# Performance work log

Hardware: AMD Instinct MI355X
Metric: run time of the kernel (lower is better)

The kernel has to match this reference:

```python
import jax, jax.numpy as jnp
import numpy as np

N_NODES = 50000


def _sage_conv(x, src, dst, W_l, b_l, W_r):
    # PyG SAGEConv (aggr='mean'): out = lin_l(mean_{j in N(i)} x_j) + lin_r(x_i)
    # lin_l has bias, lin_r has no bias.
    neigh_sum = jax.ops.segment_sum(x[src], dst, num_segments=N_NODES)  # [N, F]
    deg = jax.ops.segment_sum(jnp.ones_like(dst, dtype=x.dtype), dst, num_segments=N_NODES)
    neigh_mean = neigh_sum / jnp.maximum(deg, 1.0)[:, None]
    return neigh_mean @ W_l.T + b_l + x @ W_r.T


def setup_inputs() -> dict:
    key = jax.random.key(0)
    ks = jax.random.split(key, 8)
    D, H, C = 768, 128, 4
    x = jax.random.normal(ks[0], (N_NODES, D), dtype=jnp.float32)
    edge_index = jax.random.randint(ks[1], (2, 800000), 0, N_NODES, dtype=jnp.int64)
    s1 = 1.0 / np.sqrt(D)
    s2 = 1.0 / np.sqrt(H)
    return {
        "x": x,
        "edge_index": edge_index,
        "W1_l": jax.random.uniform(ks[2], (H, D), jnp.float32, -s1, s1),
        "b1_l": jnp.zeros((H,), jnp.float32),
        "W1_r": jax.random.uniform(ks[3], (H, D), jnp.float32, -s1, s1),
        "W2_l": jax.random.uniform(ks[4], (C, H), jnp.float32, -s2, s2),
        "b2_l": jnp.zeros((C,), jnp.float32),
        "W2_r": jax.random.uniform(ks[5], (C, H), jnp.float32, -s2, s2),
    }


def reference(x, edge_index, W1_l, b1_l, W1_r, W2_l, b2_l, W2_r):
    src, dst = edge_index[0], edge_index[1]
    h = jax.nn.relu(_sage_conv(x, src, dst, W1_l, b1_l, W1_r))  # [N, H]
    out = _sage_conv(h, src, dst, W2_l, b2_l, W2_r)  # [N, C]
    return out
```

## Files before the change

### kernel.cpp

```cpp
#include <hip/hip_runtime.h>


typedef __bf16 bf16x8 __attribute__((ext_vector_type(8)));
typedef float  f32x4  __attribute__((ext_vector_type(4)));

__device__ __forceinline__ float bf16_lo(uint32_t w) {
    union { uint32_t u; float f; } c; c.u = w << 16; return c.f;
}
__device__ __forceinline__ float bf16_hi(uint32_t w) {
    union { uint32_t u; float f; } c; c.u = w & 0xffff0000u; return c.f;
}

__global__ __launch_bounds__(256)
void convert_w(const float* __restrict__ W1l, const float* __restrict__ W1r,
               __bf16* __restrict__ Wb)
{
    int i = blockIdx.x * 256 + threadIdx.x;
    if (i >= 256 * 768) return;
    int n = i / 768, k = i - n * 768;
    float v = (n < 128) ? W1l[n * 768 + k] : W1r[(n - 128) * 768 + k];
    Wb[i] = (__bf16)v;
}

__global__ __launch_bounds__(512)
void gemm_bf16(const float* __restrict__ A, const __bf16* __restrict__ Bw,
               __bf16* __restrict__ Cb, int M)
{
    constexpr int LDK = 72;
    __shared__ __bf16 As[64][LDK];
    __shared__ __bf16 Bs[256][LDK];
    const int bm   = blockIdx.x * 64;
    const int tid  = threadIdx.x;
    const int lane = tid & 63;
    const int wave = tid >> 6;
    const int wr = wave >> 2, wc = wave & 3;
    const int l15 = lane & 15;
    const int lk  = lane >> 4;

    f32x4 acc[2][4] = {};
    float4 apref[2];
    bf16x8 bpref[4];

    const int arow = tid >> 3;
    const int akc  = (tid & 7) << 3;

    auto load_tile = [&](int k0) {
        if (bm + arow < M) {
            const float* src = A + (size_t)(bm + arow) * 768 + k0 + akc;
            apref[0] = *(const float4*)src;
            apref[1] = *(const float4*)(src + 4);
        } else {
            apref[0] = make_float4(0.f, 0.f, 0.f, 0.f);
            apref[1] = make_float4(0.f, 0.f, 0.f, 0.f);
        }
        #pragma unroll
        for (int it = 0; it < 4; ++it) {
            int v = it * 512 + tid;
            int row = v >> 3, kc = (v & 7) << 3;
            bpref[it] = *(const bf16x8*)(Bw + (size_t)row * 768 + k0 + kc);
        }
    };

    load_tile(0);
    for (int kt = 0; kt < 12; ++kt) {
        if (kt) __syncthreads();
        {
            float4 f0 = apref[0], f1 = apref[1];
            bf16x8 b;
            b[0] = (__bf16)f0.x; b[1] = (__bf16)f0.y;
            b[2] = (__bf16)f0.z; b[3] = (__bf16)f0.w;
            b[4] = (__bf16)f1.x; b[5] = (__bf16)f1.y;
            b[6] = (__bf16)f1.z; b[7] = (__bf16)f1.w;
            *(bf16x8*)&As[arow][akc] = b;
        }
        #pragma unroll
        for (int it = 0; it < 4; ++it) {
            int v = it * 512 + tid;
            int row = v >> 3, kc = (v & 7) << 3;
            *(bf16x8*)&Bs[row][kc] = bpref[it];
        }
        __syncthreads();
        if (kt < 11) load_tile((kt + 1) * 64);

        #pragma unroll
        for (int ks = 0; ks < 2; ++ks) {
            int koff = ks * 32 + lk * 8;
            bf16x8 af[2], bfr[4];
            #pragma unroll
            for (int i = 0; i < 2; ++i)
                af[i] = *(const bf16x8*)&As[wr * 32 + i * 16 + l15][koff];
            #pragma unroll
            for (int j = 0; j < 4; ++j)
                bfr[j] = *(const bf16x8*)&Bs[wc * 64 + j * 16 + l15][koff];
            #pragma unroll
            for (int i = 0; i < 2; ++i)
                #pragma unroll
                for (int j = 0; j < 4; ++j)
                    acc[i][j] = __builtin_amdgcn_mfma_f32_16x16x32_bf16(
                        af[i], bfr[j], acc[i][j], 0, 0, 0);
        }
    }

    #pragma unroll
    for (int i = 0; i < 2; ++i)
        #pragma unroll
        for (int j = 0; j < 4; ++j)
            #pragma unroll
            for (int v = 0; v < 4; ++v) {
                int row = bm + wr * 32 + i * 16 + lk * 4 + v;
                int col = wc * 64 + j * 16 + l15;
                if (row < M) Cb[(size_t)row * 256 + col] = (__bf16)acc[i][j][v];
            }
}

__global__ __launch_bounds__(256)
void zero_deg(int* __restrict__ deg, int N)
{
    int i = blockIdx.x * 256 + threadIdx.x;
    if (i < N) deg[i] = 0;
}

__global__ __launch_bounds__(256)
void csr_count(const int* __restrict__ ei, int* __restrict__ deg, int E)
{
    int e = blockIdx.x * 256 + threadIdx.x;
    if (e >= E) return;
    atomicAdd(&deg[ei[E + e]], 1);
}

__global__ __launch_bounds__(1024)
void scan1(const int* __restrict__ deg, int* __restrict__ row_ptr,
           int* __restrict__ partials, int N)
{
    __shared__ int buf[1024];
    int i = blockIdx.x * 1024 + threadIdx.x;
    int v = (i < N) ? deg[i] : 0;
    int val = v;
    buf[threadIdx.x] = val;
    __syncthreads();
    for (int off = 1; off < 1024; off <<= 1) {
        int t = (threadIdx.x >= (unsigned)off) ? buf[threadIdx.x - off] : 0;
        __syncthreads();
        val += t;
        buf[threadIdx.x] = val;
        __syncthreads();
    }
    if (i < N) row_ptr[i] = val - v;
    if (threadIdx.x == 1023) partials[blockIdx.x] = val;
}

__global__ __launch_bounds__(64)
void scan2(int* __restrict__ partials, int nb, int* __restrict__ row_ptr,
           int N, int E)
{
    int lane = threadIdx.x;
    int v = (lane < nb) ? partials[lane] : 0;
    int s = v;
    #pragma unroll
    for (int off = 1; off < 64; off <<= 1) {
        int t = __shfl_up(s, off);
        if (lane >= off) s += t;
    }
    if (lane < nb) partials[lane] = s - v;
    if (lane == 0) row_ptr[N] = E;
}

__global__ __launch_bounds__(1024)
void scan3(int* __restrict__ row_ptr, int* __restrict__ cursor,
           const int* __restrict__ partials, int N)
{
    int i = blockIdx.x * 1024 + threadIdx.x;
    if (i >= N) return;
    int v = row_ptr[i] + partials[blockIdx.x];
    row_ptr[i] = v;
    cursor[i]  = v;
}

__global__ __launch_bounds__(256)
void csr_fill(const int* __restrict__ ei, int* __restrict__ cursor,
              int* __restrict__ csr_src, int E)
{
    int e = blockIdx.x * 256 + threadIdx.x;
    if (e >= E) return;
    int src = ei[e];
    int dst = ei[E + e];
    int pos = atomicAdd(&cursor[dst], 1);
    csr_src[pos] = src;
}

__global__ __launch_bounds__(256)
void sage1_fused(const int* __restrict__ row_ptr, const int* __restrict__ csr_src,
                 const __bf16* __restrict__ pq, const float* __restrict__ b1,
                 const float* __restrict__ W2l, const float* __restrict__ W2r,
                 float* __restrict__ r, float* __restrict__ s, int N)
{
    __shared__ float Wl[512], Wr[512];
    for (int i = threadIdx.x; i < 512; i += 256) {
        Wl[i] = W2l[i];
        Wr[i] = W2r[i];
    }
    __syncthreads();

    int wid  = threadIdx.x >> 6;
    int lane = threadIdx.x & 63;
    int g = lane >> 4;
    int l = lane & 15;
    int n = blockIdx.x * 4 + wid;
    if (n >= N) return;
    int beg = row_ptr[n], end = row_ptr[n + 1];

    float acc8[8] = {};
    for (int eb = beg; eb < end; eb += 64) {
        int cnt = min(64, end - eb);
        int id = (eb + lane < end) ? csr_src[eb + lane] : 0;
        for (int t = 0; t < cnt; t += 4) {
            int src = __shfl(id, t + g);
            if (t + g < cnt) {
                uint4 w = *(const uint4*)(pq + (size_t)src * 256 + l * 8);
                acc8[0] += bf16_lo(w.x); acc8[1] += bf16_hi(w.x);
                acc8[2] += bf16_lo(w.y); acc8[3] += bf16_hi(w.y);
                acc8[4] += bf16_lo(w.z); acc8[5] += bf16_hi(w.z);
                acc8[6] += bf16_lo(w.w); acc8[7] += bf16_hi(w.w);
            }
        }
    }
    #pragma unroll
    for (int c = 0; c < 8; ++c) {
        acc8[c] += __shfl_xor(acc8[c], 16);
        acc8[c] += __shfl_xor(acc8[c], 32);
    }

    float inv = 1.0f / fmaxf((float)(end - beg), 1.0f);
    uint4  qw  = *(const uint4*)(pq + (size_t)n * 256 + 128 + l * 8);
    float4 bv0 = *(const float4*)(b1 + l * 8);
    float4 bv1 = *(const float4*)(b1 + l * 8 + 4);
    float h[8];
    h[0] = fmaxf(acc8[0] * inv + bv0.x + bf16_lo(qw.x), 0.f);
    h[1] = fmaxf(acc8[1] * inv + bv0.y + bf16_hi(qw.x), 0.f);
    h[2] = fmaxf(acc8[2] * inv + bv0.z + bf16_lo(qw.y), 0.f);
    h[3] = fmaxf(acc8[3] * inv + bv0.w + bf16_hi(qw.y), 0.f);
    h[4] = fmaxf(acc8[4] * inv + bv1.x + bf16_lo(qw.z), 0.f);
    h[5] = fmaxf(acc8[5] * inv + bv1.y + bf16_hi(qw.z), 0.f);
    h[6] = fmaxf(acc8[6] * inv + bv1.z + bf16_lo(qw.w), 0.f);
    h[7] = fmaxf(acc8[7] * inv + bv1.w + bf16_hi(qw.w), 0.f);

    float part[8];
    #pragma unroll
    for (int c = 0; c < 4; ++c) {
        float pl = 0.f, pr = 0.f;
        #pragma unroll
        for (int j = 0; j < 8; ++j) {
            pl = fmaf(h[j], Wl[c * 128 + l * 8 + j], pl);
            pr = fmaf(h[j], Wr[c * 128 + l * 8 + j], pr);
        }
        part[c] = pl; part[4 + c] = pr;
    }
    #pragma unroll
    for (int off = 8; off; off >>= 1)
        #pragma unroll
        for (int c = 0; c < 8; ++c)
            part[c] += __shfl_xor(part[c], off);
    if (lane == 0) {
        *(float4*)(r + (size_t)n * 4) = make_float4(part[0], part[1], part[2], part[3]);
        *(float4*)(s + (size_t)n * 4) = make_float4(part[4], part[5], part[6], part[7]);
    }
}

__global__ __launch_bounds__(256)
void sage2_gather(const int* __restrict__ row_ptr, const int* __restrict__ csr_src,
                  const float* __restrict__ r, const float* __restrict__ s,
                  const float* __restrict__ b2, float* __restrict__ out, int N)
{
    int t = blockIdx.x * 256 + threadIdx.x;
    if (t >= N * 4) return;
    int n = t >> 2, c = t & 3;
    int beg = row_ptr[n], end = row_ptr[n + 1];
    float acc = 0.f;
    for (int e = beg; e < end; ++e)
        acc += r[(size_t)csr_src[e] * 4 + c];
    out[t] = acc / fmaxf((float)(end - beg), 1.0f) + b2[c] + s[t];
}

extern "C" void kernel_launch(void* const* d_in, const int* in_sizes, int n_in,
                              void* d_out, int out_size, void* d_ws, size_t ws_size,
                              hipStream_t stream)
{
    const float* x   = (const float*)d_in[0];
    const int*   ei  = (const int*)d_in[1];
    const float* W1l = (const float*)d_in[2];
    const float* b1l = (const float*)d_in[3];
    const float* W1r = (const float*)d_in[4];
    const float* W2l = (const float*)d_in[5];
    const float* b2l = (const float*)d_in[6];
    const float* W2r = (const float*)d_in[7];
    float* out = (float*)d_out;

    const int N = in_sizes[0] / 768;
    const int E = in_sizes[1] / 2;
    const int NB = (N + 1023) / 1024;

    char* ws = (char*)d_ws;
    size_t off = 0;
    auto alloc = [&](size_t bytes) -> void* {
        void* pp = ws + off;
        off += (bytes + 255) & ~(size_t)255;
        return pp;
    };
    __bf16* pq      = (__bf16*)alloc((size_t)N * 256 * 2);
    float*  r       = (float*)alloc((size_t)N * 4 * 4);
    float*  s       = (float*)alloc((size_t)N * 4 * 4);
    __bf16* Wb      = (__bf16*)alloc((size_t)256 * 768 * 2);
    int*    deg     = (int*)alloc((size_t)N * 4);
    int*    row_ptr = (int*)alloc((size_t)(N + 1) * 4);
    int*    cursor  = (int*)alloc((size_t)N * 4);
    int*    csr_src = (int*)alloc((size_t)E * 4);
    int*    partials= (int*)alloc((size_t)64 * 4);

    convert_w<<<(256 * 768 + 255) / 256, 256, 0, stream>>>(W1l, W1r, Wb);
    gemm_bf16<<<(N + 63) / 64, 512, 0, stream>>>(x, Wb, pq, N);

    zero_deg<<<(N + 255) / 256, 256, 0, stream>>>(deg, N);
    csr_count<<<(E + 255) / 256, 256, 0, stream>>>(ei, deg, E);
    scan1<<<NB, 1024, 0, stream>>>(deg, row_ptr, partials, N);
    scan2<<<1, 64, 0, stream>>>(partials, NB, row_ptr, N, E);
    scan3<<<NB, 1024, 0, stream>>>(row_ptr, cursor, partials, N);
    csr_fill<<<(E + 255) / 256, 256, 0, stream>>>(ei, cursor, csr_src, E);

    sage1_fused<<<(N + 3) / 4, 256, 0, stream>>>(row_ptr, csr_src, pq, b1l,
                                                 W2l, W2r, r, s, N);

    sage2_gather<<<(N * 4 + 255) / 256, 256, 0, stream>>>(row_ptr, csr_src, r, s, b2l, out, N);
}
```

Baseline: 222.4 us.

## Pre-pack W1 in MFMA layout, drop B LDS staging, widen gather rows

The weight conversion kernel now writes W1 in a packed fragment-friendly layout. The GEMM loads B fragments directly from global memory instead of staging them through shared memory, which removes 37 KB of LDS and the per-tile B stores. The degree zeroing is merged into the prep kernel to save a launch. The layer-1 gather now uses 8 lanes per edge covering 128 features with two 16-byte loads each, so a wave handles 8 edges per step instead of 4, at the cost of more registers.

```diff
diff --git a/kernel.cpp b/kernel.cpp
--- a/kernel.cpp
+++ b/kernel.cpp
@@ -12,23 +12,24 @@
 }
 
 __global__ __launch_bounds__(256)
-void convert_w(const float* __restrict__ W1l, const float* __restrict__ W1r,
-               __bf16* __restrict__ Wb)
+void prep(const float* __restrict__ W1l, const float* __restrict__ W1r,
+          __bf16* __restrict__ Bp, int* __restrict__ deg, int N)
 {
     int i = blockIdx.x * 256 + threadIdx.x;
-    if (i >= 256 * 768) return;
-    int n = i / 768, k = i - n * 768;
-    float v = (n < 128) ? W1l[n * 768 + k] : W1r[(n - 128) * 768 + k];
-    Wb[i] = (__bf16)v;
+    if (i < N) deg[i] = 0;
+    if (i < 256 * 768) {
+        int col = i / 768, k = i - col * 768;
+        float v = (col < 128) ? W1l[col * 768 + k] : W1r[(col - 128) * 768 + k];
+        Bp[((k >> 3) << 11) + (col << 3) + (k & 7)] = (__bf16)v;
+    }
 }
 
 __global__ __launch_bounds__(512)
-void gemm_bf16(const float* __restrict__ A, const __bf16* __restrict__ Bw,
+void gemm_bf16(const float* __restrict__ A, const __bf16* __restrict__ Bp,
                __bf16* __restrict__ Cb, int M)
 {
     constexpr int LDK = 72;
     __shared__ __bf16 As[64][LDK];
-    __shared__ __bf16 Bs[256][LDK];
     const int bm   = blockIdx.x * 64;
     const int tid  = threadIdx.x;
     const int lane = tid & 63;
@@ -39,12 +40,12 @@
 
     f32x4 acc[2][4] = {};
     float4 apref[2];
-    bf16x8 bpref[4];
 
     const int arow = tid >> 3;
     const int akc  = (tid & 7) << 3;
-
-    auto load_tile = [&](int k0) {
+    const __bf16* bbase = Bp + ((size_t)(wc * 64 + l15) << 3) + ((size_t)lk << 11);
+
+    auto load_A = [&](int k0) {
         if (bm + arow < M) {
             const float* src = A + (size_t)(bm + arow) * 768 + k0 + akc;
             apref[0] = *(const float4*)src;
@@ -53,15 +54,9 @@
             apref[0] = make_float4(0.f, 0.f, 0.f, 0.f);
             apref[1] = make_float4(0.f, 0.f, 0.f, 0.f);
         }
-        #pragma unroll
-        for (int it = 0; it < 4; ++it) {
-            int v = it * 512 + tid;
-            int row = v >> 3, kc = (v & 7) << 3;
-            bpref[it] = *(const bf16x8*)(Bw + (size_t)row * 768 + k0 + kc);
-        }
     };
 
-    load_tile(0);
+    load_A(0);
     for (int kt = 0; kt < 12; ++kt) {
         if (kt) __syncthreads();
         {
@@ -73,31 +68,30 @@
             b[6] = (__bf16)f1.z; b[7] = (__bf16)f1.w;
             *(bf16x8*)&As[arow][akc] = b;
         }
-        #pragma unroll
-        for (int it = 0; it < 4; ++it) {
-            int v = it * 512 + tid;
-            int row = v >> 3, kc = (v & 7) << 3;
-            *(bf16x8*)&Bs[row][kc] = bpref[it];
-        }
         __syncthreads();
-        if (kt < 11) load_tile((kt + 1) * 64);
+        if (kt < 11) load_A((kt + 1) * 64);
+
+        bf16x8 bcur[2][4];
+        #pragma unroll
+        for (int ks = 0; ks < 2; ++ks)
+            #pragma unroll
+            for (int j = 0; j < 4; ++j)
+                bcur[ks][j] = *(const bf16x8*)(bbase +
+                    (((size_t)(kt * 8 + ks * 4) << 11) + ((size_t)j << 7)));
 
         #pragma unroll
         for (int ks = 0; ks < 2; ++ks) {
             int koff = ks * 32 + lk * 8;
-            bf16x8 af[2], bfr[4];
+            bf16x8 af[2];
             #pragma unroll
             for (int i = 0; i < 2; ++i)
                 af[i] = *(const bf16x8*)&As[wr * 32 + i * 16 + l15][koff];
-            #pragma unroll
-            for (int j = 0; j < 4; ++j)
-                bfr[j] = *(const bf16x8*)&Bs[wc * 64 + j * 16 + l15][koff];
             #pragma unroll
             for (int i = 0; i < 2; ++i)
                 #pragma unroll
                 for (int j = 0; j < 4; ++j)
                     acc[i][j] = __builtin_amdgcn_mfma_f32_16x16x32_bf16(
-                        af[i], bfr[j], acc[i][j], 0, 0, 0);
+                        af[i], bcur[ks][j], acc[i][j], 0, 0, 0);
         }
     }
 
@@ -111,13 +105,6 @@
                 int col = wc * 64 + j * 16 + l15;
                 if (row < M) Cb[(size_t)row * 256 + col] = (__bf16)acc[i][j][v];
             }
-}
-
-__global__ __launch_bounds__(256)
-void zero_deg(int* __restrict__ deg, int N)
-{
-    int i = blockIdx.x * 256 + threadIdx.x;
-    if (i < N) deg[i] = 0;
 }
 
 __global__ __launch_bounds__(256)
@@ -203,46 +190,65 @@
 
     int wid  = threadIdx.x >> 6;
     int lane = threadIdx.x & 63;
-    int g = lane >> 4;
-    int l = lane & 15;
+    int g = lane >> 3;
+    int l = lane & 7;
     int n = blockIdx.x * 4 + wid;
     if (n >= N) return;
     int beg = row_ptr[n], end = row_ptr[n + 1];
 
-    float acc8[8] = {};
+    float a0[8] = {}, a1[8] = {};
     for (int eb = beg; eb < end; eb += 64) {
         int cnt = min(64, end - eb);
         int id = (eb + lane < end) ? csr_src[eb + lane] : 0;
-        for (int t = 0; t < cnt; t += 4) {
+        for (int t = 0; t < cnt; t += 8) {
             int src = __shfl(id, t + g);
             if (t + g < cnt) {
-                uint4 w = *(const uint4*)(pq + (size_t)src * 256 + l * 8);
-                acc8[0] += bf16_lo(w.x); acc8[1] += bf16_hi(w.x);
-                acc8[2] += bf16_lo(w.y); acc8[3] += bf16_hi(w.y);
-                acc8[4] += bf16_lo(w.z); acc8[5] += bf16_hi(w.z);
-                acc8[6] += bf16_lo(w.w); acc8[7] += bf16_hi(w.w);
+                const __bf16* row = pq + (size_t)src * 256;
+                uint4 w0 = *(const uint4*)(row + l * 8);
+                uint4 w1 = *(const uint4*)(row + 64 + l * 8);
+                a0[0] += bf16_lo(w0.x); a0[1] += bf16_hi(w0.x);
+                a0[2] += bf16_lo(w0.y); a0[3] += bf16_hi(w0.y);
+                a0[4] += bf16_lo(w0.z); a0[5] += bf16_hi(w0.z);
+                a0[6] += bf16_lo(w0.w); a0[7] += bf16_hi(w0.w);
+                a1[0] += bf16_lo(w1.x); a1[1] += bf16_hi(w1.x);
+                a1[2] += bf16_lo(w1.y); a1[3] += bf16_hi(w1.y);
+                a1[4] += bf16_lo(w1.z); a1[5] += bf16_hi(w1.z);
+                a1[6] += bf16_lo(w1.w); a1[7] += bf16_hi(w1.w);
             }
         }
     }
     #pragma unroll
     for (int c = 0; c < 8; ++c) {
-        acc8[c] += __shfl_xor(acc8[c], 16);
-        acc8[c] += __shfl_xor(acc8[c], 32);
+        a0[c] += __shfl_xor(a0[c], 8);  a1[c] += __shfl_xor(a1[c], 8);
+        a0[c] += __shfl_xor(a0[c], 16); a1[c] += __shfl_xor(a1[c], 16);
+        a0[c] += __shfl_xor(a0[c], 32); a1[c] += __shfl_xor(a1[c], 32);
     }
 
     float inv = 1.0f / fmaxf((float)(end - beg), 1.0f);
-    uint4  qw  = *(const uint4*)(pq + (size_t)n * 256 + 128 + l * 8);
-    float4 bv0 = *(const float4*)(b1 + l * 8);
-    float4 bv1 = *(const float4*)(b1 + l * 8 + 4);
-    float h[8];
-    h[0] = fmaxf(acc8[0] * inv + bv0.x + bf16_lo(qw.x), 0.f);
-    h[1] = fmaxf(acc8[1] * inv + bv0.y + bf16_hi(qw.x), 0.f);
-    h[2] = fmaxf(acc8[2] * inv + bv0.z + bf16_lo(qw.y), 0.f);
-    h[3] = fmaxf(acc8[3] * inv + bv0.w + bf16_hi(qw.y), 0.f);
-    h[4] = fmaxf(acc8[4] * inv + bv1.x + bf16_lo(qw.z), 0.f);
-    h[5] = fmaxf(acc8[5] * inv + bv1.y + bf16_hi(qw.z), 0.f);
-    h[6] = fmaxf(acc8[6] * inv + bv1.z + bf16_lo(qw.w), 0.f);
-    h[7] = fmaxf(acc8[7] * inv + bv1.w + bf16_hi(qw.w), 0.f);
+    const __bf16* qrow = pq + (size_t)n * 256 + 128;
+    uint4  qw0 = *(const uint4*)(qrow + l * 8);
+    uint4  qw1 = *(const uint4*)(qrow + 64 + l * 8);
+    float4 bv00 = *(const float4*)(b1 + l * 8);
+    float4 bv01 = *(const float4*)(b1 + l * 8 + 4);
+    float4 bv10 = *(const float4*)(b1 + 64 + l * 8);
+    float4 bv11 = *(const float4*)(b1 + 64 + l * 8 + 4);
+    float h0[8], h1[8];
+    h0[0] = fmaxf(a0[0] * inv + bv00.x + bf16_lo(qw0.x), 0.f);
+    h0[1] = fmaxf(a0[1] * inv + bv00.y + bf16_hi(qw0.x), 0.f);
+    h0[2] = fmaxf(a0[2] * inv + bv00.z + bf16_lo(qw0.y), 0.f);
+    h0[3] = fmaxf(a0[3] * inv + bv00.w + bf16_hi(qw0.y), 0.f);
+    h0[4] = fmaxf(a0[4] * inv + bv01.x + bf16_lo(qw0.z), 0.f);
+    h0[5] = fmaxf(a0[5] * inv + bv01.y + bf16_hi(qw0.z), 0.f);
+    h0[6] = fmaxf(a0[6] * inv + bv01.z + bf16_lo(qw0.w), 0.f);
+    h0[7] = fmaxf(a0[7] * inv + bv01.w + bf16_hi(qw0.w), 0.f);
+    h1[0] = fmaxf(a1[0] * inv + bv10.x + bf16_lo(qw1.x), 0.f);
+    h1[1] = fmaxf(a1[1] * inv + bv10.y + bf16_hi(qw1.x), 0.f);
+    h1[2] = fmaxf(a1[2] * inv + bv10.z + bf16_lo(qw1.y), 0.f);
+    h1[3] = fmaxf(a1[3] * inv + bv10.w + bf16_hi(qw1.y), 0.f);
+    h1[4] = fmaxf(a1[4] * inv + bv11.x + bf16_lo(qw1.z), 0.f);
+    h1[5] = fmaxf(a1[5] * inv + bv11.y + bf16_hi(qw1.z), 0.f);
+    h1[6] = fmaxf(a1[6] * inv + bv11.z + bf16_lo(qw1.w), 0.f);
+    h1[7] = fmaxf(a1[7] * inv + bv11.w + bf16_hi(qw1.w), 0.f);
 
     float part[8];
     #pragma unroll
@@ -250,13 +256,15 @@
         float pl = 0.f, pr = 0.f;
         #pragma unroll
         for (int j = 0; j < 8; ++j) {
-            pl = fmaf(h[j], Wl[c * 128 + l * 8 + j], pl);
-            pr = fmaf(h[j], Wr[c * 128 + l * 8 + j], pr);
+            pl = fmaf(h0[j], Wl[c * 128 + l * 8 + j], pl);
+            pl = fmaf(h1[j], Wl[c * 128 + 64 + l * 8 + j], pl);
+            pr = fmaf(h0[j], Wr[c * 128 + l * 8 + j], pr);
+            pr = fmaf(h1[j], Wr[c * 128 + 64 + l * 8 + j], pr);
         }
         part[c] = pl; part[4 + c] = pr;
     }
     #pragma unroll
-    for (int off = 8; off; off >>= 1)
+    for (int off = 4; off; off >>= 1)
         #pragma unroll
         for (int c = 0; c < 8; ++c)
             part[c] += __shfl_xor(part[c], off);
@@ -309,17 +317,17 @@
     __bf16* pq      = (__bf16*)alloc((size_t)N * 256 * 2);
     float*  r       = (float*)alloc((size_t)N * 4 * 4);
     float*  s       = (float*)alloc((size_t)N * 4 * 4);
-    __bf16* Wb      = (__bf16*)alloc((size_t)256 * 768 * 2);
+    __bf16* Bp      = (__bf16*)alloc((size_t)256 * 768 * 2);
     int*    deg     = (int*)alloc((size_t)N * 4);
     int*    row_ptr = (int*)alloc((size_t)(N + 1) * 4);
     int*    cursor  = (int*)alloc((size_t)N * 4);
     int*    csr_src = (int*)alloc((size_t)E * 4);
     int*    partials= (int*)alloc((size_t)64 * 4);
 
-    convert_w<<<(256 * 768 + 255) / 256, 256, 0, stream>>>(W1l, W1r, Wb);
-    gemm_bf16<<<(N + 63) / 64, 512, 0, stream>>>(x, Wb, pq, N);
-
-    zero_deg<<<(N + 255) / 256, 256, 0, stream>>>(deg, N);
+    prep<<<(256 * 768 + 255) / 256, 256, 0, stream>>>(W1l, W1r, Bp, deg, N);
+
+    gemm_bf16<<<(N + 63) / 64, 512, 0, stream>>>(x, Bp, pq, N);
+
     csr_count<<<(E + 255) / 256, 256, 0, stream>>>(ei, deg, E);
     scan1<<<NB, 1024, 0, stream>>>(deg, row_ptr, partials, N);
     scan2<<<1, 64, 0, stream>>>(partials, NB, row_ptr, N, E);
```

New measurement: 221.6 us. No clear change (-0.3%).
